# Kernel optimization log

Hardware: AMD Instinct MI355X
Metric: run time of the kernel (lower is better)

The kernel has to match this reference:

```python
import jax, jax.numpy as jnp
import numpy as np

D = 1024  # bilinear_dim
IN_A = 1024
IN_B = 1024

def setup_inputs() -> dict:
    key = jax.random.key(0)
    ks = jax.random.split(key, 8)
    B, La, Lb = 64, 256, 256
    sa = 1.0 / np.sqrt(IN_A)
    sb = 1.0 / np.sqrt(IN_B)
    sd = 1.0 / np.sqrt(D)
    return {
        "a": jax.random.normal(ks[0], (B, La, IN_A), dtype=jnp.float32),
        "b": jax.random.normal(ks[1], (B, Lb, IN_B), dtype=jnp.float32),
        "Wa": jax.random.uniform(ks[2], (IN_A, D), jnp.float32, -sa, sa),
        "ba": jax.random.uniform(ks[3], (D,), jnp.float32, -sa, sa),
        "Wb": jax.random.uniform(ks[4], (IN_B, D), jnp.float32, -sb, sb),
        "bb": jax.random.uniform(ks[5], (D,), jnp.float32, -sb, sb),
        "w": jax.random.uniform(ks[6], (D,), jnp.float32, -sd, sd),
        "wbias": jax.random.uniform(ks[7], (), jnp.float32, -sd, sd),
    }

def reference(a, b, Wa, ba, Wb, bb, w, wbias):
    # Linear projections (dropout inactive at inference)
    pa = a @ Wa + ba          # (B, La, D)
    pb = b @ Wb + bb          # (B, Lb, D)
    # Fused bilinear score: sum_d w[d]*pa[b,i,d]*pb[b,j,d] + wbias
    # (equivalent to materializing (B,La,Lb,D) outer product then Linear(D->1))
    scores = jnp.einsum('bid,bjd->bij', pa * w, pb) + wbias  # (B, La, Lb)
    B, La, Lb = scores.shape
    norm = jax.nn.softmax(scores.reshape(B, La * Lb), axis=1)
    return norm.reshape(B, La, Lb)
```

## Files before the change

kernel.cpp:

```cpp
#include <hip/hip_runtime.h>
#include <hip/hip_bf16.h>

typedef __attribute__((ext_vector_type(8))) short bf16x8;
typedef __attribute__((ext_vector_type(4))) float f32x4;

#define K_DIM 1024
#define N_PROJ 1024
#define M_PROJ 16384
#define NBATCH 64
#define SEQ 256

static __device__ inline unsigned short bf16_bits(float f) {
    __hip_bfloat16 h = __float2bfloat16(f);
    return *reinterpret_cast<unsigned short*>(&h);
}

#define GLOAD16(g, l) __builtin_amdgcn_global_load_lds(                          \
    (__attribute__((address_space(1))) void*)(g),                                \
    (__attribute__((address_space(3))) void*)(l), 16, 0, 0)

__global__ __launch_bounds__(256) void f32_to_bf16(const float* __restrict__ in,
                                                   unsigned short* __restrict__ out,
                                                   int n8)
{
    int i = blockIdx.x * 256 + threadIdx.x;
    if (i >= n8) return;
    const float4* p = reinterpret_cast<const float4*>(in) + (size_t)i * 2;
    float4 v0 = p[0], v1 = p[1];
    unsigned short u[8];
    u[0] = bf16_bits(v0.x); u[1] = bf16_bits(v0.y); u[2] = bf16_bits(v0.z); u[3] = bf16_bits(v0.w);
    u[4] = bf16_bits(v1.x); u[5] = bf16_bits(v1.y); u[6] = bf16_bits(v1.z); u[7] = bf16_bits(v1.w);
    *reinterpret_cast<uint4*>(out + (size_t)i * 8) = *reinterpret_cast<uint4*>(u);
}

__global__ __launch_bounds__(256) void transpose_w(const float* __restrict__ W,
                                                   unsigned short* __restrict__ Wt)
{
    __shared__ float t[64][65];
    const int k0 = blockIdx.x * 64;
    const int n0 = blockIdx.y * 64;
    const int tr = threadIdx.x >> 4;
    const int tc = (threadIdx.x & 15) * 4;

#pragma unroll
    for (int r = 0; r < 4; ++r) {
        float4 v = *reinterpret_cast<const float4*>(&W[(size_t)(k0 + tr + r * 16) * N_PROJ + n0 + tc]);
        t[tr + r * 16][tc + 0] = v.x;
        t[tr + r * 16][tc + 1] = v.y;
        t[tr + r * 16][tc + 2] = v.z;
        t[tr + r * 16][tc + 3] = v.w;
    }
    __syncthreads();
#pragma unroll
    for (int r = 0; r < 4; ++r) {
        const int on = tr + r * 16;
        unsigned short u[4];
#pragma unroll
        for (int i = 0; i < 4; ++i) u[i] = bf16_bits(t[tc + i][on]);
        *reinterpret_cast<ushort4*>(&Wt[(size_t)(n0 + on) * K_DIM + k0 + tc]) =
            *reinterpret_cast<ushort4*>(u);
    }
}

__global__ __launch_bounds__(512, 2) void proj_gemm256(
    const __hip_bfloat16* __restrict__ A,
    const __hip_bfloat16* __restrict__ Wt,
    const float* __restrict__ bias,
    const float* __restrict__ scale,
    __hip_bfloat16* __restrict__ out,
    int use_scale)
{
    __shared__ __align__(16) unsigned short lds[2][4][128 * 64];

    const int tid  = threadIdx.x;
    const int lane = tid & 63;
    const int w    = tid >> 6;
    const int wr   = w >> 2;
    const int wc   = w & 3;
    const int m0 = blockIdx.x * 256;
    const int n0 = blockIdx.y * 256;

    const int c1 = w * 128 + lane, c2 = c1 + 64;
    const int r1 = c1 >> 3, r2 = c2 >> 3;
    const int k1 = (c1 & 7) ^ (r1 & 7);
    const int k2 = (c2 & 7) ^ (r2 & 7);

    const int lrow = lane & 15;
    const int kq0  = (((lane >> 4) + 0) ^ (lane & 7)) * 16;
    const int kq1  = (((lane >> 4) + 4) ^ (lane & 7)) * 16;

#define STG(SRC, RB, KB, BUF, REG)                                               \
    {                                                                            \
        GLOAD16((SRC) + (size_t)((RB) + r1) * K_DIM + (KB) + k1 * 8,             \
                (char*)(&lds[BUF][REG][0]) + w * 2048);                          \
        GLOAD16((SRC) + (size_t)((RB) + r2) * K_DIM + (KB) + k2 * 8,             \
                (char*)(&lds[BUF][REG][0]) + w * 2048 + 1024);                   \
    }

    f32x4 acc[8][4];
#pragma unroll
    for (int i = 0; i < 8; ++i)
#pragma unroll
        for (int j = 0; j < 4; ++j) acc[i][j] = f32x4{0.f, 0.f, 0.f, 0.f};

    STG(A,  m0,       0, 0, 0); STG(A,  m0 + 128,  0, 0, 1);
    STG(Wt, n0,       0, 0, 2); STG(Wt, n0 + 128,  0, 0, 3);
    STG(A,  m0,      64, 1, 0); STG(A,  m0 + 128, 64, 1, 1);
    asm volatile("s_waitcnt vmcnt(4)" ::: "memory");
    __builtin_amdgcn_sched_barrier(0);
    __builtin_amdgcn_s_barrier();

#define KTILE(CUR, NXT, T)                                                       \
    {                                                                            \
        const int kb1 = (((T) + 1) & 15) << 6;                                   \
        const int kb2 = (((T) + 2) & 15) << 6;                                   \
        const char* Ab = (const char*)(&lds[CUR][wr][0]);                        \
        const char* Bb = (const char*)(&lds[CUR][2 + (wc >> 1)][0])              \
                         + (wc & 1) * 8192;                                      \
        bf16x8 af[4][2], bfr[4][2];                                              \
               \
        _Pragma("unroll")                                                        \
        for (int mi = 0; mi < 4; ++mi) {                                         \
            af[mi][0] = *(const bf16x8*)(Ab + mi * 2048 + lrow * 128 + kq0);     \
            af[mi][1] = *(const bf16x8*)(Ab + mi * 2048 + lrow * 128 + kq1);     \
        }                                                                        \
        _Pragma("unroll")                                                        \
        for (int nj = 0; nj < 2; ++nj) {                                         \
            bfr[nj][0] = *(const bf16x8*)(Bb + nj * 2048 + lrow * 128 + kq0);    \
            bfr[nj][1] = *(const bf16x8*)(Bb + nj * 2048 + lrow * 128 + kq1);    \
        }                                                                        \
        STG(Wt, n0, kb1, NXT, 2);                                                \
        __builtin_amdgcn_sched_barrier(0);                                       \
        __builtin_amdgcn_s_barrier();                                            \
        asm volatile("s_waitcnt lgkmcnt(0)" ::: "memory");                       \
        __builtin_amdgcn_sched_barrier(0);                                       \
        __builtin_amdgcn_s_setprio(1);                                           \
        _Pragma("unroll")                                                        \
        for (int mi = 0; mi < 4; ++mi)                                           \
            _Pragma("unroll")                                                    \
            for (int nj = 0; nj < 2; ++nj) {                                     \
                acc[mi][nj] = __builtin_amdgcn_mfma_f32_16x16x32_bf16(           \
                    af[mi][0], bfr[nj][0], acc[mi][nj], 0, 0, 0);                \
                acc[mi][nj] = __builtin_amdgcn_mfma_f32_16x16x32_bf16(           \
                    af[mi][1], bfr[nj][1], acc[mi][nj], 0, 0, 0);                \
            }                                                                    \
        __builtin_amdgcn_s_setprio(0);                                           \
        __builtin_amdgcn_sched_barrier(0);                                       \
        __builtin_amdgcn_s_barrier();                                            \
                          \
        _Pragma("unroll")                                                        \
        for (int nj = 2; nj < 4; ++nj) {                                         \
            bfr[nj][0] = *(const bf16x8*)(Bb + nj * 2048 + lrow * 128 + kq0);    \
            bfr[nj][1] = *(const bf16x8*)(Bb + nj * 2048 + lrow * 128 + kq1);    \
        }                                                                        \
        STG(Wt, n0 + 128, kb1, NXT, 3);                                          \
        __builtin_amdgcn_sched_barrier(0);                                       \
        __builtin_amdgcn_s_barrier();                                            \
        asm volatile("s_waitcnt lgkmcnt(0)" ::: "memory");                       \
        __builtin_amdgcn_sched_barrier(0);                                       \
        __builtin_amdgcn_s_setprio(1);                                           \
        _Pragma("unroll")                                                        \
        for (int mi = 0; mi < 4; ++mi)                                           \
            _Pragma("unroll")                                                    \
            for (int nj = 2; nj < 4; ++nj) {                                     \
                acc[mi][nj] = __builtin_amdgcn_mfma_f32_16x16x32_bf16(           \
                    af[mi][0], bfr[nj][0], acc[mi][nj], 0, 0, 0);                \
                acc[mi][nj] = __builtin_amdgcn_mfma_f32_16x16x32_bf16(           \
                    af[mi][1], bfr[nj][1], acc[mi][nj], 0, 0, 0);                \
            }                                                                    \
        __builtin_amdgcn_s_setprio(0);                                           \
        __builtin_amdgcn_sched_barrier(0);                                       \
        __builtin_amdgcn_s_barrier();                                            \
                                \
        _Pragma("unroll")                                                        \
        for (int mi = 0; mi < 4; ++mi) {                                         \
            af[mi][0] = *(const bf16x8*)(Ab + 8192 + mi * 2048 + lrow * 128 + kq0);\
            af[mi][1] = *(const bf16x8*)(Ab + 8192 + mi * 2048 + lrow * 128 + kq1);\
        }                                                                        \
        __builtin_amdgcn_sched_barrier(0);                                       \
        __builtin_amdgcn_s_barrier();                                            \
        asm volatile("s_waitcnt lgkmcnt(0)" ::: "memory");                       \
        __builtin_amdgcn_sched_barrier(0);                                       \
        __builtin_amdgcn_s_setprio(1);                                           \
        _Pragma("unroll")                                                        \
        for (int mi = 0; mi < 4; ++mi)                                           \
            _Pragma("unroll")                                                    \
            for (int nj = 0; nj < 2; ++nj) {                                     \
                acc[4 + mi][nj] = __builtin_amdgcn_mfma_f32_16x16x32_bf16(       \
                    af[mi][0], bfr[nj][0], acc[4 + mi][nj], 0, 0, 0);            \
                acc[4 + mi][nj] = __builtin_amdgcn_mfma_f32_16x16x32_bf16(       \
                    af[mi][1], bfr[nj][1], acc[4 + mi][nj], 0, 0, 0);            \
            }                                                                    \
        __builtin_amdgcn_s_setprio(0);                                           \
        __builtin_amdgcn_sched_barrier(0);                                       \
        __builtin_amdgcn_s_barrier();                                            \
         \
        STG(A, m0,       kb2, CUR, 0);                                           \
        STG(A, m0 + 128, kb2, CUR, 1);                                           \
        __builtin_amdgcn_sched_barrier(0);                                       \
        __builtin_amdgcn_s_barrier();                                            \
        __builtin_amdgcn_s_setprio(1);                                           \
        _Pragma("unroll")                                                        \
        for (int mi = 0; mi < 4; ++mi)                                           \
            _Pragma("unroll")                                                    \
            for (int nj = 2; nj < 4; ++nj) {                                     \
                acc[4 + mi][nj] = __builtin_amdgcn_mfma_f32_16x16x32_bf16(       \
                    af[mi][0], bfr[nj][0], acc[4 + mi][nj], 0, 0, 0);            \
                acc[4 + mi][nj] = __builtin_amdgcn_mfma_f32_16x16x32_bf16(       \
                    af[mi][1], bfr[nj][1], acc[4 + mi][nj], 0, 0, 0);            \
            }                                                                    \
        __builtin_amdgcn_s_setprio(0);                                           \
        asm volatile("s_waitcnt vmcnt(4)" ::: "memory");                         \
        __builtin_amdgcn_sched_barrier(0);                                       \
        __builtin_amdgcn_s_barrier();                                            \
    }

    for (int tt = 0; tt < 8; ++tt) {
        const int t0 = tt * 2;
        KTILE(0, 1, t0);
        KTILE(1, 0, t0 + 1);
    }
#undef KTILE
#undef STG

#pragma unroll
    for (int nj = 0; nj < 4; ++nj) {
        const int col = n0 + wc * 64 + nj * 16 + lrow;
        const float bc = bias[col];
        const float sc = use_scale ? scale[col] : 1.0f;
#pragma unroll
        for (int mi8 = 0; mi8 < 8; ++mi8) {
            const int rowoff = (mi8 >> 2) * 64 + (mi8 & 3) * 16;
#pragma unroll
            for (int r = 0; r < 4; ++r) {
                const int row = m0 + wr * 128 + rowoff + (lane >> 4) * 4 + r;
                out[(size_t)row * N_PROJ + col] = __float2bfloat16((acc[mi8][nj][r] + bc) * sc);
            }
        }
    }
}

__global__ __launch_bounds__(256) void score_gemm(const __hip_bfloat16* __restrict__ PA,
                                                  const __hip_bfloat16* __restrict__ PB,
                                                  const float* __restrict__ wbias,
                                                  float* __restrict__ out,
                                                  float* __restrict__ partials)
{
    __shared__ __align__(16) unsigned short As[128][32];
    __shared__ __align__(16) unsigned short Bs[128][32];
    __shared__ float psum[4];

    const int tid  = threadIdx.x;
    const int lane = tid & 63;
    const int wave = tid >> 6;
    const int b  = blockIdx.z;
    const int i0 = blockIdx.x * 128;
    const int j0 = blockIdx.y * 128;
    const int wr = (wave >> 1) * 64;
    const int wc = (wave & 1) * 64;

    const __hip_bfloat16* Arow = PA + (size_t)(b * SEQ + i0) * K_DIM;
    const __hip_bfloat16* Brow = PB + (size_t)(b * SEQ + j0) * K_DIM;

    f32x4 acc[4][4];
#pragma unroll
    for (int i = 0; i < 4; ++i)
#pragma unroll
        for (int j = 0; j < 4; ++j) acc[i][j] = f32x4{0.f, 0.f, 0.f, 0.f};

    const int lrow = lane & 15;
    const int kq   = (lane >> 4) * 8;

    for (int k0 = 0; k0 < K_DIM; k0 += 32) {
        __syncthreads();
#pragma unroll
        for (int it = 0; it < 2; ++it) {
            const int chunk = (it * 4 + wave) * 64 + lane;
            const int row = chunk >> 2;
            const int col = (chunk & 3) * 8;
            GLOAD16(Arow + (size_t)row * K_DIM + k0 + col,
                    reinterpret_cast<char*>(&As[0][0]) + (it * 4 + wave) * 1024);
        }
#pragma unroll
        for (int it = 0; it < 2; ++it) {
            const int chunk = (it * 4 + wave) * 64 + lane;
            const int row = chunk >> 2;
            const int col = (chunk & 3) * 8;
            GLOAD16(Brow + (size_t)row * K_DIM + k0 + col,
                    reinterpret_cast<char*>(&Bs[0][0]) + (it * 4 + wave) * 1024);
        }
        __syncthreads();

        bf16x8 af[4], bfr[4];
#pragma unroll
        for (int f = 0; f < 4; ++f) {
            af[f]  = *reinterpret_cast<const bf16x8*>(&As[wr + f * 16 + lrow][kq]);
            bfr[f] = *reinterpret_cast<const bf16x8*>(&Bs[wc + f * 16 + lrow][kq]);
        }
#pragma unroll
        for (int i = 0; i < 4; ++i)
#pragma unroll
            for (int j = 0; j < 4; ++j)
                acc[i][j] = __builtin_amdgcn_mfma_f32_16x16x32_bf16(af[i], bfr[j], acc[i][j], 0, 0, 0);
    }

    const float wb = *wbias;
    float lsum = 0.f;
#pragma unroll
    for (int j = 0; j < 4; ++j) {
        const int col = j0 + wc + j * 16 + (lane & 15);
#pragma unroll
        for (int i = 0; i < 4; ++i) {
#pragma unroll
            for (int r = 0; r < 4; ++r) {
                const int row = i0 + wr + i * 16 + (lane >> 4) * 4 + r;
                const float e = __expf(acc[i][j][r] + wb);
                lsum += e;
                out[(size_t)b * (SEQ * SEQ) + (size_t)row * SEQ + col] = e;
            }
        }
    }
#pragma unroll
    for (int off = 32; off; off >>= 1) lsum += __shfl_down(lsum, off);
    if (lane == 0) psum[wave] = lsum;
    __syncthreads();
    if (tid == 0)
        partials[b * 4 + blockIdx.x * 2 + blockIdx.y] =
            (psum[0] + psum[1]) + (psum[2] + psum[3]);
}

__global__ __launch_bounds__(1024) void normalize_k(float* __restrict__ s,
                                                    const float* __restrict__ partials)
{
    const int b    = blockIdx.x >> 2;
    const int part = blockIdx.x & 3;
    const float inv = 1.0f / (((partials[b * 4 + 0] + partials[b * 4 + 1]) +
                               partials[b * 4 + 2]) + partials[b * 4 + 3]);
    float4* p4 = reinterpret_cast<float4*>(s + (size_t)b * (SEQ * SEQ));
    const int base = part * 4096;
#pragma unroll
    for (int it = 0; it < 4; ++it) {
        const int i = base + it * 1024 + threadIdx.x;
        float4 v = p4[i];
        v.x *= inv; v.y *= inv; v.z *= inv; v.w *= inv;
        p4[i] = v;
    }
}

extern "C" void kernel_launch(void* const* d_in, const int* in_sizes, int n_in,
                              void* d_out, int out_size, void* d_ws, size_t ws_size,
                              hipStream_t stream)
{
    const float* a     = (const float*)d_in[0];
    const float* b     = (const float*)d_in[1];
    const float* Wa    = (const float*)d_in[2];
    const float* ba    = (const float*)d_in[3];
    const float* Wb    = (const float*)d_in[4];
    const float* bb    = (const float*)d_in[5];
    const float* w     = (const float*)d_in[6];
    const float* wbias = (const float*)d_in[7];
    float* out = (float*)d_out;

    char* wsb = (char*)d_ws;
    unsigned short* xbf = (unsigned short*)(wsb);
    unsigned short* Wt  = (unsigned short*)(wsb + (size_t)33554432);
    __hip_bfloat16* paw = (__hip_bfloat16*)(wsb + (size_t)35651584);
    __hip_bfloat16* pb  = (__hip_bfloat16*)(wsb + (size_t)69206016);
    float* partials     = (float*)(wsb);

    const int n8 = (M_PROJ * K_DIM) / 8;
    const dim3 cgrid(n8 / 256);
    const dim3 tgrid(16, 16);
    const dim3 pgrid(M_PROJ / 256, N_PROJ / 256);

    transpose_w<<<tgrid, 256, 0, stream>>>(Wa, Wt);
    f32_to_bf16<<<cgrid, 256, 0, stream>>>(a, xbf, n8);
    proj_gemm256<<<pgrid, 512, 0, stream>>>((const __hip_bfloat16*)xbf, (const __hip_bfloat16*)Wt,
                                            ba, w, paw, 1);
    transpose_w<<<tgrid, 256, 0, stream>>>(Wb, Wt);
    f32_to_bf16<<<cgrid, 256, 0, stream>>>(b, xbf, n8);
    proj_gemm256<<<pgrid, 512, 0, stream>>>((const __hip_bfloat16*)xbf, (const __hip_bfloat16*)Wt,
                                            bb, w, pb, 0);

    const dim3 sgrid(SEQ / 128, SEQ / 128, NBATCH);
    score_gemm<<<sgrid, 256, 0, stream>>>(paw, pb, wbias, out, partials);

    normalize_k<<<NBATCH * 4, 1024, 0, stream>>>(out, partials);
}
```

Before: 154.0 us.

## Fuse fp32-to-bf16 activation conversion into projection GEMM loads

Removes the standalone f32_to_bf16 kernels. The projection GEMM now loads fp32 activations into registers, converts them to bf16 and writes them into swizzled LDS, prefetching two k-tiles ahead. This avoids writing and re-reading a 32MB bf16 copy twice. MFMA operand order is swapped so each lane holds four consecutive columns, which enables vectorized ushort4/float4 epilogue stores in both the projection and score kernels. The cost is more VGPR pressure from the register staging and a full vmcnt(0) wait per tile.

```diff
diff --git a/kernel.cpp b/kernel.cpp
--- a/kernel.cpp
+++ b/kernel.cpp
@@ -18,20 +18,6 @@
 #define GLOAD16(g, l) __builtin_amdgcn_global_load_lds(                          \
     (__attribute__((address_space(1))) void*)(g),                                \
     (__attribute__((address_space(3))) void*)(l), 16, 0, 0)
-
-__global__ __launch_bounds__(256) void f32_to_bf16(const float* __restrict__ in,
-                                                   unsigned short* __restrict__ out,
-                                                   int n8)
-{
-    int i = blockIdx.x * 256 + threadIdx.x;
-    if (i >= n8) return;
-    const float4* p = reinterpret_cast<const float4*>(in) + (size_t)i * 2;
-    float4 v0 = p[0], v1 = p[1];
-    unsigned short u[8];
-    u[0] = bf16_bits(v0.x); u[1] = bf16_bits(v0.y); u[2] = bf16_bits(v0.z); u[3] = bf16_bits(v0.w);
-    u[4] = bf16_bits(v1.x); u[5] = bf16_bits(v1.y); u[6] = bf16_bits(v1.z); u[7] = bf16_bits(v1.w);
-    *reinterpret_cast<uint4*>(out + (size_t)i * 8) = *reinterpret_cast<uint4*>(u);
-}
 
 __global__ __launch_bounds__(256) void transpose_w(const float* __restrict__ W,
                                                    unsigned short* __restrict__ Wt)
@@ -63,7 +49,7 @@
 }
 
 __global__ __launch_bounds__(512, 2) void proj_gemm256(
-    const __hip_bfloat16* __restrict__ A,
+    const float* __restrict__ A,
     const __hip_bfloat16* __restrict__ Wt,
     const float* __restrict__ bias,
     const float* __restrict__ scale,
@@ -85,40 +71,80 @@
     const int k1 = (c1 & 7) ^ (r1 & 7);
     const int k2 = (c2 & 7) ^ (r2 & 7);
 
+    const int areg   = w >> 2;
+    const int arow_l = lane >> 3;
+    const int akc    = (lane & 7) * 2;
+    const int aphysb = ((lane & 7) ^ (arow_l & 7)) * 16;
+    const int atrow  = (w >> 2) * 128 + (w & 3) * 32 + arow_l;
+
     const int lrow = lane & 15;
     const int kq0  = (((lane >> 4) + 0) ^ (lane & 7)) * 16;
     const int kq1  = (((lane >> 4) + 4) ^ (lane & 7)) * 16;
 
-#define STG(SRC, RB, KB, BUF, REG)                                               \
+#define STGB(RB, KB, BUF, REG)                                                   \
     {                                                                            \
-        GLOAD16((SRC) + (size_t)((RB) + r1) * K_DIM + (KB) + k1 * 8,             \
+        GLOAD16(Wt + (size_t)((RB) + r1) * K_DIM + (KB) + k1 * 8,                \
                 (char*)(&lds[BUF][REG][0]) + w * 2048);                          \
-        GLOAD16((SRC) + (size_t)((RB) + r2) * K_DIM + (KB) + k2 * 8,             \
+        GLOAD16(Wt + (size_t)((RB) + r2) * K_DIM + (KB) + k2 * 8,                \
                 (char*)(&lds[BUF][REG][0]) + w * 2048 + 1024);                   \
     }
 
+#define ALOAD(TT)                                                                \
+    {                                                                            \
+        const float* ap_ = A + (size_t)(m0 + atrow) * K_DIM                      \
+                           + (((TT) & 15) << 6) + akc * 4;                       \
+        _Pragma("unroll")                                                        \
+        for (int j_ = 0; j_ < 4; ++j_) {                                         \
+            rs[j_ * 2 + 0] = *(const float4*)(ap_ + (size_t)j_ * 8 * K_DIM);     \
+            rs[j_ * 2 + 1] = *(const float4*)(ap_ + (size_t)j_ * 8 * K_DIM + 4); \
+        }                                                                        \
+    }
+
+#define AWRITE(BUF)                                                              \
+    {                                                                            \
+        _Pragma("unroll")                                                        \
+        for (int j_ = 0; j_ < 4; ++j_) {                                         \
+            unsigned short u_[8];                                                \
+            u_[0] = bf16_bits(rs[2*j_].x);   u_[1] = bf16_bits(rs[2*j_].y);      \
+            u_[2] = bf16_bits(rs[2*j_].z);   u_[3] = bf16_bits(rs[2*j_].w);      \
+            u_[4] = bf16_bits(rs[2*j_+1].x); u_[5] = bf16_bits(rs[2*j_+1].y);    \
+            u_[6] = bf16_bits(rs[2*j_+1].z); u_[7] = bf16_bits(rs[2*j_+1].w);    \
+            *(uint4*)((char*)(&lds[BUF][areg][0])                                \
+                      + ((w & 3) * 32 + arow_l + j_ * 8) * 128 + aphysb)         \
+                = *(uint4*)u_;                                                   \
+        }                                                                        \
+    }
+
+    float4 rs[8];
     f32x4 acc[8][4];
 #pragma unroll
     for (int i = 0; i < 8; ++i)
 #pragma unroll
         for (int j = 0; j < 4; ++j) acc[i][j] = f32x4{0.f, 0.f, 0.f, 0.f};
 
-    STG(A,  m0,       0, 0, 0); STG(A,  m0 + 128,  0, 0, 1);
-    STG(Wt, n0,       0, 0, 2); STG(Wt, n0 + 128,  0, 0, 3);
-    STG(A,  m0,      64, 1, 0); STG(A,  m0 + 128, 64, 1, 1);
+    ALOAD(0);
+    STGB(n0,       0, 0, 2);
+    STGB(n0 + 128, 0, 0, 3);
     asm volatile("s_waitcnt vmcnt(4)" ::: "memory");
+    __builtin_amdgcn_sched_barrier(0);
+    AWRITE(0);
+    ALOAD(1);
+    asm volatile("s_waitcnt vmcnt(8)" ::: "memory");
+    asm volatile("s_waitcnt lgkmcnt(0)" ::: "memory");
     __builtin_amdgcn_sched_barrier(0);
     __builtin_amdgcn_s_barrier();
 
 #define KTILE(CUR, NXT, T)                                                       \
     {                                                                            \
         const int kb1 = (((T) + 1) & 15) << 6;                                   \
-        const int kb2 = (((T) + 2) & 15) << 6;                                   \
         const char* Ab = (const char*)(&lds[CUR][wr][0]);                        \
         const char* Bb = (const char*)(&lds[CUR][2 + (wc >> 1)][0])              \
                          + (wc & 1) * 8192;                                      \
         bf16x8 af[4][2], bfr[4][2];                                              \
-               \
+        \
+        asm volatile("s_waitcnt vmcnt(0)" ::: "memory");                         \
+        __builtin_amdgcn_sched_barrier(0);                                       \
+        AWRITE(NXT);                                                             \
         _Pragma("unroll")                                                        \
         for (int mi = 0; mi < 4; ++mi) {                                         \
             af[mi][0] = *(const bf16x8*)(Ab + mi * 2048 + lrow * 128 + kq0);     \
@@ -129,7 +155,7 @@
             bfr[nj][0] = *(const bf16x8*)(Bb + nj * 2048 + lrow * 128 + kq0);    \
             bfr[nj][1] = *(const bf16x8*)(Bb + nj * 2048 + lrow * 128 + kq1);    \
         }                                                                        \
-        STG(Wt, n0, kb1, NXT, 2);                                                \
+        STGB(n0, kb1, NXT, 2);                                                   \
         __builtin_amdgcn_sched_barrier(0);                                       \
         __builtin_amdgcn_s_barrier();                                            \
         asm volatile("s_waitcnt lgkmcnt(0)" ::: "memory");                       \
@@ -140,20 +166,20 @@
             _Pragma("unroll")                                                    \
             for (int nj = 0; nj < 2; ++nj) {                                     \
                 acc[mi][nj] = __builtin_amdgcn_mfma_f32_16x16x32_bf16(           \
-                    af[mi][0], bfr[nj][0], acc[mi][nj], 0, 0, 0);                \
+                    bfr[nj][0], af[mi][0], acc[mi][nj], 0, 0, 0);                \
                 acc[mi][nj] = __builtin_amdgcn_mfma_f32_16x16x32_bf16(           \
-                    af[mi][1], bfr[nj][1], acc[mi][nj], 0, 0, 0);                \
+                    bfr[nj][1], af[mi][1], acc[mi][nj], 0, 0, 0);                \
             }                                                                    \
         __builtin_amdgcn_s_setprio(0);                                           \
         __builtin_amdgcn_sched_barrier(0);                                       \
         __builtin_amdgcn_s_barrier();                                            \
-                          \
+                                          \
         _Pragma("unroll")                                                        \
         for (int nj = 2; nj < 4; ++nj) {                                         \
             bfr[nj][0] = *(const bf16x8*)(Bb + nj * 2048 + lrow * 128 + kq0);    \
             bfr[nj][1] = *(const bf16x8*)(Bb + nj * 2048 + lrow * 128 + kq1);    \
         }                                                                        \
-        STG(Wt, n0 + 128, kb1, NXT, 3);                                          \
+        STGB(n0 + 128, kb1, NXT, 3);                                             \
         __builtin_amdgcn_sched_barrier(0);                                       \
         __builtin_amdgcn_s_barrier();                                            \
         asm volatile("s_waitcnt lgkmcnt(0)" ::: "memory");                       \
@@ -164,19 +190,20 @@
             _Pragma("unroll")                                                    \
             for (int nj = 2; nj < 4; ++nj) {                                     \
                 acc[mi][nj] = __builtin_amdgcn_mfma_f32_16x16x32_bf16(           \
-                    af[mi][0], bfr[nj][0], acc[mi][nj], 0, 0, 0);                \
+                    bfr[nj][0], af[mi][0], acc[mi][nj], 0, 0, 0);                \
                 acc[mi][nj] = __builtin_amdgcn_mfma_f32_16x16x32_bf16(           \
-                    af[mi][1], bfr[nj][1], acc[mi][nj], 0, 0, 0);                \
+                    bfr[nj][1], af[mi][1], acc[mi][nj], 0, 0, 0);                \
             }                                                                    \
         __builtin_amdgcn_s_setprio(0);                                           \
         __builtin_amdgcn_sched_barrier(0);                                       \
         __builtin_amdgcn_s_barrier();                                            \
-                                \
+                          \
         _Pragma("unroll")                                                        \
         for (int mi = 0; mi < 4; ++mi) {                                         \
             af[mi][0] = *(const bf16x8*)(Ab + 8192 + mi * 2048 + lrow * 128 + kq0);\
             af[mi][1] = *(const bf16x8*)(Ab + 8192 + mi * 2048 + lrow * 128 + kq1);\
         }                                                                        \
+        ALOAD((T) + 2);                                                          \
         __builtin_amdgcn_sched_barrier(0);                                       \
         __builtin_amdgcn_s_barrier();                                            \
         asm volatile("s_waitcnt lgkmcnt(0)" ::: "memory");                       \
@@ -187,30 +214,26 @@
             _Pragma("unroll")                                                    \
             for (int nj = 0; nj < 2; ++nj) {                                     \
                 acc[4 + mi][nj] = __builtin_amdgcn_mfma_f32_16x16x32_bf16(       \
-                    af[mi][0], bfr[nj][0], acc[4 + mi][nj], 0, 0, 0);            \
+                    bfr[nj][0], af[mi][0], acc[4 + mi][nj], 0, 0, 0);            \
                 acc[4 + mi][nj] = __builtin_amdgcn_mfma_f32_16x16x32_bf16(       \
-                    af[mi][1], bfr[nj][1], acc[4 + mi][nj], 0, 0, 0);            \
+                    bfr[nj][1], af[mi][1], acc[4 + mi][nj], 0, 0, 0);            \
             }                                                                    \
         __builtin_amdgcn_s_setprio(0);                                           \
         __builtin_amdgcn_sched_barrier(0);                                       \
         __builtin_amdgcn_s_barrier();                                            \
-         \
-        STG(A, m0,       kb2, CUR, 0);                                           \
-        STG(A, m0 + 128, kb2, CUR, 1);                                           \
-        __builtin_amdgcn_sched_barrier(0);                                       \
-        __builtin_amdgcn_s_barrier();                                            \
+               \
         __builtin_amdgcn_s_setprio(1);                                           \
         _Pragma("unroll")                                                        \
         for (int mi = 0; mi < 4; ++mi)                                           \
             _Pragma("unroll")                                                    \
             for (int nj = 2; nj < 4; ++nj) {                                     \
                 acc[4 + mi][nj] = __builtin_amdgcn_mfma_f32_16x16x32_bf16(       \
-                    af[mi][0], bfr[nj][0], acc[4 + mi][nj], 0, 0, 0);            \
+                    bfr[nj][0], af[mi][0], acc[4 + mi][nj], 0, 0, 0);            \
                 acc[4 + mi][nj] = __builtin_amdgcn_mfma_f32_16x16x32_bf16(       \
-                    af[mi][1], bfr[nj][1], acc[4 + mi][nj], 0, 0, 0);            \
+                    bfr[nj][1], af[mi][1], acc[4 + mi][nj], 0, 0, 0);            \
             }                                                                    \
         __builtin_amdgcn_s_setprio(0);                                           \
-        asm volatile("s_waitcnt vmcnt(4)" ::: "memory");                         \
+        asm volatile("s_waitcnt vmcnt(8)" ::: "memory");                         \
         __builtin_amdgcn_sched_barrier(0);                                       \
         __builtin_amdgcn_s_barrier();                                            \
     }
@@ -220,22 +243,29 @@
         KTILE(0, 1, t0);
         KTILE(1, 0, t0 + 1);
     }
+    asm volatile("s_waitcnt vmcnt(0)" ::: "memory");
+
 #undef KTILE
-#undef STG
+#undef AWRITE
+#undef ALOAD
+#undef STGB
 
 #pragma unroll
     for (int nj = 0; nj < 4; ++nj) {
-        const int col = n0 + wc * 64 + nj * 16 + lrow;
-        const float bc = bias[col];
-        const float sc = use_scale ? scale[col] : 1.0f;
+        const int nb = n0 + wc * 64 + nj * 16 + (lane >> 4) * 4;
+        const float4 bc = *(const float4*)&bias[nb];
+        float4 sc;
+        if (use_scale) sc = *(const float4*)&scale[nb];
+        else           sc = float4{1.f, 1.f, 1.f, 1.f};
 #pragma unroll
         for (int mi8 = 0; mi8 < 8; ++mi8) {
-            const int rowoff = (mi8 >> 2) * 64 + (mi8 & 3) * 16;
-#pragma unroll
-            for (int r = 0; r < 4; ++r) {
-                const int row = m0 + wr * 128 + rowoff + (lane >> 4) * 4 + r;
-                out[(size_t)row * N_PROJ + col] = __float2bfloat16((acc[mi8][nj][r] + bc) * sc);
-            }
+            const int m = m0 + wr * 128 + (mi8 >> 2) * 64 + (mi8 & 3) * 16 + lrow;
+            unsigned short u[4];
+            u[0] = bf16_bits((acc[mi8][nj][0] + bc.x) * sc.x);
+            u[1] = bf16_bits((acc[mi8][nj][1] + bc.y) * sc.y);
+            u[2] = bf16_bits((acc[mi8][nj][2] + bc.z) * sc.z);
+            u[3] = bf16_bits((acc[mi8][nj][3] + bc.w) * sc.w);
+            *(ushort4*)&out[(size_t)m * N_PROJ + nb] = *(ushort4*)u;
         }
     }
 }
@@ -301,23 +331,24 @@
         for (int i = 0; i < 4; ++i)
 #pragma unroll
             for (int j = 0; j < 4; ++j)
-                acc[i][j] = __builtin_amdgcn_mfma_f32_16x16x32_bf16(af[i], bfr[j], acc[i][j], 0, 0, 0);
+                acc[i][j] = __builtin_amdgcn_mfma_f32_16x16x32_bf16(bfr[j], af[i], acc[i][j], 0, 0, 0);
     }
 
     const float wb = *wbias;
     float lsum = 0.f;
 #pragma unroll
-    for (int j = 0; j < 4; ++j) {
-        const int col = j0 + wc + j * 16 + (lane & 15);
-#pragma unroll
-        for (int i = 0; i < 4; ++i) {
-#pragma unroll
-            for (int r = 0; r < 4; ++r) {
-                const int row = i0 + wr + i * 16 + (lane >> 4) * 4 + r;
-                const float e = __expf(acc[i][j][r] + wb);
-                lsum += e;
-                out[(size_t)b * (SEQ * SEQ) + (size_t)row * SEQ + col] = e;
-            }
+    for (int ii = 0; ii < 4; ++ii) {
+        const int i = i0 + wr + ii * 16 + lrow;
+#pragma unroll
+        for (int jj = 0; jj < 4; ++jj) {
+            const int jb = j0 + wc + jj * 16 + (lane >> 4) * 4;
+            float4 e;
+            e.x = __expf(acc[ii][jj][0] + wb);
+            e.y = __expf(acc[ii][jj][1] + wb);
+            e.z = __expf(acc[ii][jj][2] + wb);
+            e.w = __expf(acc[ii][jj][3] + wb);
+            lsum += (e.x + e.y) + (e.z + e.w);
+            *(float4*)&out[(size_t)b * (SEQ * SEQ) + (size_t)i * SEQ + jb] = e;
         }
     }
 #pragma unroll
@@ -362,25 +393,18 @@
     float* out = (float*)d_out;
 
     char* wsb = (char*)d_ws;
-    unsigned short* xbf = (unsigned short*)(wsb);
-    unsigned short* Wt  = (unsigned short*)(wsb + (size_t)33554432);
-    __hip_bfloat16* paw = (__hip_bfloat16*)(wsb + (size_t)35651584);
-    __hip_bfloat16* pb  = (__hip_bfloat16*)(wsb + (size_t)69206016);
-    float* partials     = (float*)(wsb);
-
-    const int n8 = (M_PROJ * K_DIM) / 8;
-    const dim3 cgrid(n8 / 256);
+    unsigned short* Wt  = (unsigned short*)(wsb);
+    __hip_bfloat16* paw = (__hip_bfloat16*)(wsb + (size_t)2097152);
+    __hip_bfloat16* pb  = (__hip_bfloat16*)(wsb + (size_t)35651584);
+    float* partials     = (float*)(wsb + (size_t)69206016);
+
     const dim3 tgrid(16, 16);
     const dim3 pgrid(M_PROJ / 256, N_PROJ / 256);
 
     transpose_w<<<tgrid, 256, 0, stream>>>(Wa, Wt);
-    f32_to_bf16<<<cgrid, 256, 0, stream>>>(a, xbf, n8);
-    proj_gemm256<<<pgrid, 512, 0, stream>>>((const __hip_bfloat16*)xbf, (const __hip_bfloat16*)Wt,
-                                            ba, w, paw, 1);
+    proj_gemm256<<<pgrid, 512, 0, stream>>>(a, (const __hip_bfloat16*)Wt, ba, w, paw, 1);
     transpose_w<<<tgrid, 256, 0, stream>>>(Wb, Wt);
-    f32_to_bf16<<<cgrid, 256, 0, stream>>>(b, xbf, n8);
-    proj_gemm256<<<pgrid, 512, 0, stream>>>((const __hip_bfloat16*)xbf, (const __hip_bfloat16*)Wt,
-                                            bb, w, pb, 0);
+    proj_gemm256<<<pgrid, 512, 0, stream>>>(b, (const __hip_bfloat16*)Wt, bb, w, pb, 0);
 
     const dim3 sgrid(SEQ / 128, SEQ / 128, NBATCH);
     score_gemm<<<sgrid, 256, 0, stream>>>(paw, pb, wbias, out, partials);
```

Result: slower. 182.9 us (+18.7%).

## Reassociate bilinear score through precomputed Wa·diag(w)·Wbᵀ to drop one projection GEMM

Applied to the files above, without the earlier changes.

Instead of projecting both a and b with separate large GEMMs, the code precomputes the small matrix M = Wa·diag(w)·Wbᵀ and applies it to a in a single large GEMM. The score GEMM then uses raw bf16 b directly. Bias cross-terms are precomputed as per-row vectors alpha and beta plus a constant c, and added in the softmax epilogue with vectorized float4 stores. This removes roughly one large GEMM of work but adds extra bf16 rounding of M and of the intermediate product.

```diff
diff --git a/kernel.cpp b/kernel.cpp
--- a/kernel.cpp
+++ b/kernel.cpp
@@ -5,7 +5,6 @@
 typedef __attribute__((ext_vector_type(4))) float f32x4;
 
 #define K_DIM 1024
-#define N_PROJ 1024
 #define M_PROJ 16384
 #define NBATCH 64
 #define SEQ 256
@@ -19,46 +18,173 @@
     (__attribute__((address_space(1))) void*)(g),                                \
     (__attribute__((address_space(3))) void*)(l), 16, 0, 0)
 
-__global__ __launch_bounds__(256) void f32_to_bf16(const float* __restrict__ in,
+__global__ __launch_bounds__(256) void uvc_kernel(const float* __restrict__ Wa,
+                                                  const float* __restrict__ Wb,
+                                                  const float* __restrict__ w,
+                                                  const float* __restrict__ ba,
+                                                  const float* __restrict__ bb,
+                                                  float* __restrict__ u,
+                                                  float* __restrict__ v,
+                                                  float* __restrict__ c)
+{
+    __shared__ float psum[4];
+    const int p = blockIdx.x;
+    const int t = threadIdx.x;
+    const int d0 = t * 4;
+
+    float part = 0.f;
+    if (p < 1024) {
+        float4 m = *(const float4*)&Wa[(size_t)p * K_DIM + d0];
+        float4 ww = *(const float4*)&w[d0];
+        float4 bv = *(const float4*)&bb[d0];
+        part = m.x * ww.x * bv.x + m.y * ww.y * bv.y + m.z * ww.z * bv.z + m.w * ww.w * bv.w;
+    } else if (p < 2048) {
+        float4 m = *(const float4*)&Wb[(size_t)(p - 1024) * K_DIM + d0];
+        float4 ww = *(const float4*)&w[d0];
+        float4 bv = *(const float4*)&ba[d0];
+        part = m.x * ww.x * bv.x + m.y * ww.y * bv.y + m.z * ww.z * bv.z + m.w * ww.w * bv.w;
+    } else {
+        float4 ww = *(const float4*)&w[d0];
+        float4 b1 = *(const float4*)&ba[d0];
+        float4 b2 = *(const float4*)&bb[d0];
+        part = ww.x * b1.x * b2.x + ww.y * b1.y * b2.y + ww.z * b1.z * b2.z + ww.w * b1.w * b2.w;
+    }
+#pragma unroll
+    for (int off = 32; off; off >>= 1) part += __shfl_down(part, off);
+    if ((t & 63) == 0) psum[t >> 6] = part;
+    __syncthreads();
+    if (t == 0) {
+        const float s = (psum[0] + psum[1]) + (psum[2] + psum[3]);
+        if (p < 1024) u[p] = s;
+        else if (p < 2048) v[p - 1024] = s;
+        else *c = s;
+    }
+}
+
+__global__ __launch_bounds__(256) void wscale_conv(const float* __restrict__ in,
+                                                   const float* __restrict__ w,
                                                    unsigned short* __restrict__ out,
-                                                   int n8)
-{
-    int i = blockIdx.x * 256 + threadIdx.x;
-    if (i >= n8) return;
+                                                   int scale_by_w)
+{
+    const int i = blockIdx.x * 256 + threadIdx.x;
+    const int d0 = (i * 8) & (K_DIM - 1);
     const float4* p = reinterpret_cast<const float4*>(in) + (size_t)i * 2;
     float4 v0 = p[0], v1 = p[1];
-    unsigned short u[8];
-    u[0] = bf16_bits(v0.x); u[1] = bf16_bits(v0.y); u[2] = bf16_bits(v0.z); u[3] = bf16_bits(v0.w);
-    u[4] = bf16_bits(v1.x); u[5] = bf16_bits(v1.y); u[6] = bf16_bits(v1.z); u[7] = bf16_bits(v1.w);
-    *reinterpret_cast<uint4*>(out + (size_t)i * 8) = *reinterpret_cast<uint4*>(u);
-}
-
-__global__ __launch_bounds__(256) void transpose_w(const float* __restrict__ W,
-                                                   unsigned short* __restrict__ Wt)
-{
-    __shared__ float t[64][65];
-    const int k0 = blockIdx.x * 64;
-    const int n0 = blockIdx.y * 64;
-    const int tr = threadIdx.x >> 4;
-    const int tc = (threadIdx.x & 15) * 4;
-
-#pragma unroll
-    for (int r = 0; r < 4; ++r) {
-        float4 v = *reinterpret_cast<const float4*>(&W[(size_t)(k0 + tr + r * 16) * N_PROJ + n0 + tc]);
-        t[tr + r * 16][tc + 0] = v.x;
-        t[tr + r * 16][tc + 1] = v.y;
-        t[tr + r * 16][tc + 2] = v.z;
-        t[tr + r * 16][tc + 3] = v.w;
-    }
+    if (scale_by_w) {
+        float4 w0 = *(const float4*)&w[d0];
+        float4 w1 = *(const float4*)&w[d0 + 4];
+        v0.x *= w0.x; v0.y *= w0.y; v0.z *= w0.z; v0.w *= w0.w;
+        v1.x *= w1.x; v1.y *= w1.y; v1.z *= w1.z; v1.w *= w1.w;
+    }
+    unsigned short uo[8];
+    uo[0] = bf16_bits(v0.x); uo[1] = bf16_bits(v0.y); uo[2] = bf16_bits(v0.z); uo[3] = bf16_bits(v0.w);
+    uo[4] = bf16_bits(v1.x); uo[5] = bf16_bits(v1.y); uo[6] = bf16_bits(v1.z); uo[7] = bf16_bits(v1.w);
+    *reinterpret_cast<uint4*>(out + (size_t)i * 8) = *reinterpret_cast<uint4*>(uo);
+}
+
+__global__ __launch_bounds__(256) void conv_rows(const float* __restrict__ X,
+                                                 const float* __restrict__ dvec,
+                                                 unsigned short* __restrict__ out,
+                                                 float* __restrict__ rowdot)
+{
+    __shared__ float psum[4];
+    const int t = threadIdx.x;
+    const int r = blockIdx.x * 2 + (t >> 7);
+    const int c8 = (t & 127) * 8;
+
+    const float* xp = &X[(size_t)r * K_DIM + c8];
+    float4 v0 = *(const float4*)xp;
+    float4 v1 = *(const float4*)(xp + 4);
+    float4 u0 = *(const float4*)&dvec[c8];
+    float4 u1 = *(const float4*)&dvec[c8 + 4];
+    float part = v0.x * u0.x + v0.y * u0.y + v0.z * u0.z + v0.w * u0.w
+               + v1.x * u1.x + v1.y * u1.y + v1.z * u1.z + v1.w * u1.w;
+
+    unsigned short uo[8];
+    uo[0] = bf16_bits(v0.x); uo[1] = bf16_bits(v0.y); uo[2] = bf16_bits(v0.z); uo[3] = bf16_bits(v0.w);
+    uo[4] = bf16_bits(v1.x); uo[5] = bf16_bits(v1.y); uo[6] = bf16_bits(v1.z); uo[7] = bf16_bits(v1.w);
+    *reinterpret_cast<uint4*>(&out[(size_t)r * K_DIM + c8]) = *reinterpret_cast<uint4*>(uo);
+
+#pragma unroll
+    for (int off = 32; off; off >>= 1) part += __shfl_down(part, off);
+    if ((t & 63) == 0) psum[t >> 6] = part;
     __syncthreads();
-#pragma unroll
-    for (int r = 0; r < 4; ++r) {
-        const int on = tr + r * 16;
-        unsigned short u[4];
-#pragma unroll
-        for (int i = 0; i < 4; ++i) u[i] = bf16_bits(t[tc + i][on]);
-        *reinterpret_cast<ushort4*>(&Wt[(size_t)(n0 + on) * K_DIM + k0 + tc]) =
-            *reinterpret_cast<ushort4*>(u);
+    if ((t & 127) == 0) rowdot[r] = psum[(t >> 6)] + psum[(t >> 6) + 1];
+}
+
+__global__ __launch_bounds__(256) void mt_gemm(const __hip_bfloat16* __restrict__ Wb16,
+                                               const __hip_bfloat16* __restrict__ Waw,
+                                               unsigned short* __restrict__ Mt)
+{
+    __shared__ __align__(16) unsigned short As[128][32];
+    __shared__ __align__(16) unsigned short Bs[128][32];
+
+    const int tid  = threadIdx.x;
+    const int lane = tid & 63;
+    const int wave = tid >> 6;
+    const int q0 = blockIdx.x * 128;
+    const int p0 = blockIdx.y * 128;
+    const int wr = (wave >> 1) * 64;
+    const int wc = (wave & 1) * 64;
+
+    const __hip_bfloat16* Arow = Wb16 + (size_t)q0 * K_DIM;
+    const __hip_bfloat16* Brow = Waw + (size_t)p0 * K_DIM;
+
+    f32x4 acc[4][4];
+#pragma unroll
+    for (int i = 0; i < 4; ++i)
+#pragma unroll
+        for (int j = 0; j < 4; ++j) acc[i][j] = f32x4{0.f, 0.f, 0.f, 0.f};
+
+    const int lrow = lane & 15;
+    const int kq   = (lane >> 4) * 8;
+
+    for (int k0 = 0; k0 < K_DIM; k0 += 32) {
+        __syncthreads();
+#pragma unroll
+        for (int it = 0; it < 2; ++it) {
+            const int chunk = (it * 4 + wave) * 64 + lane;
+            const int row = chunk >> 2;
+            const int col = (chunk & 3) * 8;
+            GLOAD16(Arow + (size_t)row * K_DIM + k0 + col,
+                    reinterpret_cast<char*>(&As[0][0]) + (it * 4 + wave) * 1024);
+        }
+#pragma unroll
+        for (int it = 0; it < 2; ++it) {
+            const int chunk = (it * 4 + wave) * 64 + lane;
+            const int row = chunk >> 2;
+            const int col = (chunk & 3) * 8;
+            GLOAD16(Brow + (size_t)row * K_DIM + k0 + col,
+                    reinterpret_cast<char*>(&Bs[0][0]) + (it * 4 + wave) * 1024);
+        }
+        __syncthreads();
+
+        bf16x8 af[4], bfr[4];
+#pragma unroll
+        for (int f = 0; f < 4; ++f) {
+            af[f]  = *reinterpret_cast<const bf16x8*>(&As[wr + f * 16 + lrow][kq]);
+            bfr[f] = *reinterpret_cast<const bf16x8*>(&Bs[wc + f * 16 + lrow][kq]);
+        }
+#pragma unroll
+        for (int i = 0; i < 4; ++i)
+#pragma unroll
+            for (int j = 0; j < 4; ++j)
+                acc[i][j] = __builtin_amdgcn_mfma_f32_16x16x32_bf16(bfr[j], af[i], acc[i][j], 0, 0, 0);
+    }
+
+#pragma unroll
+    for (int ii = 0; ii < 4; ++ii) {
+        const int q = q0 + wr + ii * 16 + lrow;
+#pragma unroll
+        for (int jj = 0; jj < 4; ++jj) {
+            const int pb = p0 + wc + jj * 16 + (lane >> 4) * 4;
+            unsigned short uo[4];
+            uo[0] = bf16_bits(acc[ii][jj][0]);
+            uo[1] = bf16_bits(acc[ii][jj][1]);
+            uo[2] = bf16_bits(acc[ii][jj][2]);
+            uo[3] = bf16_bits(acc[ii][jj][3]);
+            *(ushort4*)&Mt[(size_t)q * K_DIM + pb] = *(ushort4*)uo;
+        }
     }
 }
 
@@ -68,7 +194,7 @@
     const float* __restrict__ bias,
     const float* __restrict__ scale,
     __hip_bfloat16* __restrict__ out,
-    int use_scale)
+    int use_bias, int use_scale)
 {
     __shared__ __align__(16) unsigned short lds[2][4][128 * 64];
 
@@ -118,7 +244,6 @@
         const char* Bb = (const char*)(&lds[CUR][2 + (wc >> 1)][0])              \
                          + (wc & 1) * 8192;                                      \
         bf16x8 af[4][2], bfr[4][2];                                              \
-               \
         _Pragma("unroll")                                                        \
         for (int mi = 0; mi < 4; ++mi) {                                         \
             af[mi][0] = *(const bf16x8*)(Ab + mi * 2048 + lrow * 128 + kq0);     \
@@ -147,7 +272,6 @@
         __builtin_amdgcn_s_setprio(0);                                           \
         __builtin_amdgcn_sched_barrier(0);                                       \
         __builtin_amdgcn_s_barrier();                                            \
-                          \
         _Pragma("unroll")                                                        \
         for (int nj = 2; nj < 4; ++nj) {                                         \
             bfr[nj][0] = *(const bf16x8*)(Bb + nj * 2048 + lrow * 128 + kq0);    \
@@ -171,7 +295,6 @@
         __builtin_amdgcn_s_setprio(0);                                           \
         __builtin_amdgcn_sched_barrier(0);                                       \
         __builtin_amdgcn_s_barrier();                                            \
-                                \
         _Pragma("unroll")                                                        \
         for (int mi = 0; mi < 4; ++mi) {                                         \
             af[mi][0] = *(const bf16x8*)(Ab + 8192 + mi * 2048 + lrow * 128 + kq0);\
@@ -194,7 +317,6 @@
         __builtin_amdgcn_s_setprio(0);                                           \
         __builtin_amdgcn_sched_barrier(0);                                       \
         __builtin_amdgcn_s_barrier();                                            \
-         \
         STG(A, m0,       kb2, CUR, 0);                                           \
         STG(A, m0 + 128, kb2, CUR, 1);                                           \
         __builtin_amdgcn_sched_barrier(0);                                       \
@@ -220,13 +342,14 @@
         KTILE(0, 1, t0);
         KTILE(1, 0, t0 + 1);
     }
+    asm volatile("s_waitcnt vmcnt(0)" ::: "memory");
 #undef KTILE
 #undef STG
 
 #pragma unroll
     for (int nj = 0; nj < 4; ++nj) {
         const int col = n0 + wc * 64 + nj * 16 + lrow;
-        const float bc = bias[col];
+        const float bc = use_bias ? bias[col] : 0.0f;
         const float sc = use_scale ? scale[col] : 1.0f;
 #pragma unroll
         for (int mi8 = 0; mi8 < 8; ++mi8) {
@@ -234,14 +357,17 @@
 #pragma unroll
             for (int r = 0; r < 4; ++r) {
                 const int row = m0 + wr * 128 + rowoff + (lane >> 4) * 4 + r;
-                out[(size_t)row * N_PROJ + col] = __float2bfloat16((acc[mi8][nj][r] + bc) * sc);
+                out[(size_t)row * K_DIM + col] = __float2bfloat16((acc[mi8][nj][r] + bc) * sc);
             }
         }
     }
 }
 
-__global__ __launch_bounds__(256) void score_gemm(const __hip_bfloat16* __restrict__ PA,
-                                                  const __hip_bfloat16* __restrict__ PB,
+__global__ __launch_bounds__(256) void score_gemm(const __hip_bfloat16* __restrict__ T,
+                                                  const __hip_bfloat16* __restrict__ Bbf,
+                                                  const float* __restrict__ alpha,
+                                                  const float* __restrict__ beta,
+                                                  const float* __restrict__ cptr,
                                                   const float* __restrict__ wbias,
                                                   float* __restrict__ out,
                                                   float* __restrict__ partials)
@@ -259,8 +385,8 @@
     const int wr = (wave >> 1) * 64;
     const int wc = (wave & 1) * 64;
 
-    const __hip_bfloat16* Arow = PA + (size_t)(b * SEQ + i0) * K_DIM;
-    const __hip_bfloat16* Brow = PB + (size_t)(b * SEQ + j0) * K_DIM;
+    const __hip_bfloat16* Arow = T + (size_t)(b * SEQ + i0) * K_DIM;
+    const __hip_bfloat16* Brow = Bbf + (size_t)(b * SEQ + j0) * K_DIM;
 
     f32x4 acc[4][4];
 #pragma unroll
@@ -301,23 +427,26 @@
         for (int i = 0; i < 4; ++i)
 #pragma unroll
             for (int j = 0; j < 4; ++j)
-                acc[i][j] = __builtin_amdgcn_mfma_f32_16x16x32_bf16(af[i], bfr[j], acc[i][j], 0, 0, 0);
-    }
-
-    const float wb = *wbias;
+                acc[i][j] = __builtin_amdgcn_mfma_f32_16x16x32_bf16(bfr[j], af[i], acc[i][j], 0, 0, 0);
+    }
+
+    const float cwb = *cptr + *wbias;
     float lsum = 0.f;
 #pragma unroll
-    for (int j = 0; j < 4; ++j) {
-        const int col = j0 + wc + j * 16 + (lane & 15);
-#pragma unroll
-        for (int i = 0; i < 4; ++i) {
-#pragma unroll
-            for (int r = 0; r < 4; ++r) {
-                const int row = i0 + wr + i * 16 + (lane >> 4) * 4 + r;
-                const float e = __expf(acc[i][j][r] + wb);
-                lsum += e;
-                out[(size_t)b * (SEQ * SEQ) + (size_t)row * SEQ + col] = e;
-            }
+    for (int ii = 0; ii < 4; ++ii) {
+        const int i = i0 + wr + ii * 16 + lrow;
+        const float av = alpha[b * SEQ + i] + cwb;
+#pragma unroll
+        for (int jj = 0; jj < 4; ++jj) {
+            const int jb = j0 + wc + jj * 16 + (lane >> 4) * 4;
+            const float4 bv = *(const float4*)&beta[b * SEQ + jb];
+            float4 e;
+            e.x = __expf(acc[ii][jj][0] + av + bv.x);
+            e.y = __expf(acc[ii][jj][1] + av + bv.y);
+            e.z = __expf(acc[ii][jj][2] + av + bv.z);
+            e.w = __expf(acc[ii][jj][3] + av + bv.w);
+            lsum += (e.x + e.y) + (e.z + e.w);
+            *(float4*)&out[(size_t)b * (SEQ * SEQ) + (size_t)i * SEQ + jb] = e;
         }
     }
 #pragma unroll
@@ -362,28 +491,32 @@
     float* out = (float*)d_out;
 
     char* wsb = (char*)d_ws;
-    unsigned short* xbf = (unsigned short*)(wsb);
-    unsigned short* Wt  = (unsigned short*)(wsb + (size_t)33554432);
-    __hip_bfloat16* paw = (__hip_bfloat16*)(wsb + (size_t)35651584);
-    __hip_bfloat16* pb  = (__hip_bfloat16*)(wsb + (size_t)69206016);
-    float* partials     = (float*)(wsb);
-
-    const int n8 = (M_PROJ * K_DIM) / 8;
-    const dim3 cgrid(n8 / 256);
-    const dim3 tgrid(16, 16);
-    const dim3 pgrid(M_PROJ / 256, N_PROJ / 256);
-
-    transpose_w<<<tgrid, 256, 0, stream>>>(Wa, Wt);
-    f32_to_bf16<<<cgrid, 256, 0, stream>>>(a, xbf, n8);
-    proj_gemm256<<<pgrid, 512, 0, stream>>>((const __hip_bfloat16*)xbf, (const __hip_bfloat16*)Wt,
-                                            ba, w, paw, 1);
-    transpose_w<<<tgrid, 256, 0, stream>>>(Wb, Wt);
-    f32_to_bf16<<<cgrid, 256, 0, stream>>>(b, xbf, n8);
-    proj_gemm256<<<pgrid, 512, 0, stream>>>((const __hip_bfloat16*)xbf, (const __hip_bfloat16*)Wt,
-                                            bb, w, pb, 0);
-
+    unsigned short* Waw   = (unsigned short*)(wsb);
+    unsigned short* Wb16  = (unsigned short*)(wsb + (size_t)2097152);
+    unsigned short* Mt    = (unsigned short*)(wsb + (size_t)4194304);
+    float* u              = (float*)(wsb + (size_t)6291456);
+    float* v              = (float*)(wsb + (size_t)6291456 + 4096);
+    float* c              = (float*)(wsb + (size_t)6291456 + 8192);
+    float* alpha          = (float*)(wsb + (size_t)6291456 + 16384);
+    float* beta           = (float*)(wsb + (size_t)6291456 + 16384 + 65536);
+    float* partials       = (float*)(wsb + (size_t)6291456 + 16384 + 131072);
+    unsigned short* ab16  = (unsigned short*)(wsb + (size_t)8388608);
+    unsigned short* Tbuf  = (unsigned short*)(wsb + (size_t)41943040);
+
+    uvc_kernel<<<2049, 256, 0, stream>>>(Wa, Wb, w, ba, bb, u, v, c);
+    wscale_conv<<<512, 256, 0, stream>>>(Wa, w, Waw, 1);
+    wscale_conv<<<512, 256, 0, stream>>>(Wb, w, Wb16, 0);
+    mt_gemm<<<dim3(8, 8), 256, 0, stream>>>((const __hip_bfloat16*)Wb16,
+                                            (const __hip_bfloat16*)Waw, Mt);
+    conv_rows<<<M_PROJ / 2, 256, 0, stream>>>(a, u, ab16, alpha);
+    const dim3 pgrid(M_PROJ / 256, K_DIM / 256);
+    proj_gemm256<<<pgrid, 512, 0, stream>>>((const __hip_bfloat16*)ab16,
+                                            (const __hip_bfloat16*)Mt,
+                                            u, u, (__hip_bfloat16*)Tbuf, 0, 0);
+    conv_rows<<<M_PROJ / 2, 256, 0, stream>>>(b, v, ab16, beta);
     const dim3 sgrid(SEQ / 128, SEQ / 128, NBATCH);
-    score_gemm<<<sgrid, 256, 0, stream>>>(paw, pb, wbias, out, partials);
-
+    score_gemm<<<sgrid, 256, 0, stream>>>((const __hip_bfloat16*)Tbuf,
+                                          (const __hip_bfloat16*)ab16,
+                                          alpha, beta, c, wbias, out, partials);
     normalize_k<<<NBATCH * 4, 1024, 0, stream>>>(out, partials);
 }
```

Measured after the change: 138.3 us. -10.2%, faster.
